# Kernel tuning notes

Measured on AMD Instinct MI355X. Metric: run time of the kernel, lower is better.

The kernel has to match this reference:

```python
import jax, jax.numpy as jnp
import numpy as np

EMBED = 768
HEADS = 12


def setup_inputs() -> dict:
    key = jax.random.key(0)
    k1, k2, k3 = jax.random.split(key, 3)
    B, N, E = 2, 2048, EMBED
    x = jax.random.normal(k1, (B, N, E), dtype=jnp.float32)
    w_qkv = jax.random.normal(k2, (3 * E, E), dtype=jnp.float32) * (1.0 / np.sqrt(E))
    b_qkv = jnp.zeros((3 * E,), dtype=jnp.float32)
    w_o = jax.random.normal(k3, (E, E), dtype=jnp.float32) * (1.0 / np.sqrt(E))
    b_o = jnp.zeros((E,), dtype=jnp.float32)
    return {"x": x, "w_qkv": w_qkv, "b_qkv": b_qkv, "w_o": w_o, "b_o": b_o}


def reference(x, w_qkv, b_qkv, w_o, b_o):
    B, N, E = x.shape
    H = HEADS
    d = E // H
    # fused qkv projection (torch Linear: x @ W^T + b)
    qkv = x @ w_qkv.T + b_qkv                       # [B, N, 3E]
    # Rearrange 'b n (h qkv e) -> b qkv h n e'
    qkv = qkv.reshape(B, N, H, 3, d).transpose(0, 3, 2, 1, 4)  # [B, 3, H, N, d]
    q, k, v = qkv[:, 0], qkv[:, 1], qkv[:, 2]       # each [B, H, N, d]
    scores = jnp.einsum("bhqd,bhkd->bhqk", q, k)    # [B, H, N, N]
    attn = jax.nn.softmax(scores / jnp.sqrt(jnp.float32(E)), axis=-1)
    ctx = jnp.einsum("bhqk,bhkd->bhqd", attn, v)    # [B, H, N, d]
    ctx = ctx.transpose(0, 2, 1, 3).reshape(B, N, E)  # 'b h n d -> b n (h d)'
    out = ctx @ w_o.T + b_o
    return out
```

## Files before the change

### kernel.cpp

```cpp
#include <hip/hip_runtime.h>

#define BB 2
#define NN 2048
#define EE 768
#define HH 12
#define DD 64
#define MM (BB*NN)
#define E3 (3*EE)
#define QSCALE 0.05205877280961602f

typedef __bf16 bf16x8 __attribute__((ext_vector_type(8)));
typedef float  f32x4  __attribute__((ext_vector_type(4)));
typedef unsigned short u16x8 __attribute__((ext_vector_type(8)));

#define MFMA(a,b,c) __builtin_amdgcn_mfma_f32_16x16x32_bf16(a,b,c,0,0,0)

__device__ __forceinline__ unsigned short f2bf(float f) {
    unsigned int u = __float_as_uint(f);
    u += 0x7FFFu + ((u >> 16) & 1u);
    return (unsigned short)(u >> 16);
}

__device__ __forceinline__ bf16x8 as_bf16x8(u16x8 v) {
    union { u16x8 u; bf16x8 b; } c; c.u = v; return c.b;
}

typedef __attribute__((address_space(3))) unsigned int as3u32;
typedef __attribute__((address_space(1))) unsigned int as1u32;
__device__ __forceinline__ void gll16(const void* g, void* l) {
    __builtin_amdgcn_global_load_lds((const as1u32*)(uintptr_t)g,
                                     (as3u32*)(unsigned int)(uintptr_t)l, 16, 0, 0);
}

#define XB4 786432
#define WQ4 442368
#define WO4 147456
__global__ __launch_bounds__(256)
void cast3(const float* __restrict__ x, const float* __restrict__ wq,
           const float* __restrict__ wo, unsigned short* __restrict__ dst) {
    int i = blockIdx.x * 256 + threadIdx.x;
    const float* src;
    int off;
    if (i < XB4)            { src = x;  off = i; }
    else if (i < XB4+WQ4)   { src = wq; off = i - XB4; }
    else                    { src = wo; off = i - XB4 - WQ4; }
    float4 v = ((const float4*)src)[off];
    ushort4 o;
    o.x = f2bf(v.x); o.y = f2bf(v.y); o.z = f2bf(v.z); o.w = f2bf(v.w);
    ((ushort4*)dst)[i] = o;
}

__global__ __launch_bounds__(256)
void gemm_qkv(const unsigned short* __restrict__ A, const unsigned short* __restrict__ W,
              const float* __restrict__ bias,
              unsigned short* __restrict__ o0, unsigned short* __restrict__ o1,
              unsigned short* __restrict__ o2)
{
    __shared__ unsigned short As[128 * 32];
    __shared__ unsigned short Bs[64 * 32];

    const int tid = threadIdx.x;
    const int l = tid & 63;
    const int w = tid >> 6;
    const int m0 = blockIdx.x * 128;
    const int c0 = blockIdx.y * 64;
    const int wm = (w >> 1) * 64;
    const int wn = (w & 1) * 32;

    const unsigned short* s_src[3];
    unsigned short* s_dst[3];
    #pragma unroll
    for (int s = 0; s < 3; ++s) {
        const int ch = 3*w + s;
        if (ch < 8) {
            s_src[s] = A + (size_t)(m0 + ch*16 + (l>>2)) * EE + (l&3)*8;
            s_dst[s] = &As[ch*512];
        } else {
            s_src[s] = W + (size_t)(c0 + (ch-8)*16 + (l>>2)) * EE + (l&3)*8;
            s_dst[s] = &Bs[(ch-8)*512];
        }
    }

    const f32x4 zero4 = {0.f, 0.f, 0.f, 0.f};
    f32x4 acc[4][2];
    #pragma unroll
    for (int i = 0; i < 4; ++i)
        #pragma unroll
        for (int j = 0; j < 2; ++j) acc[i][j] = zero4;

    for (int k0 = 0; k0 < EE; k0 += 32) {
        __syncthreads();
        #pragma unroll
        for (int s = 0; s < 3; ++s) gll16(s_src[s] + k0, s_dst[s]);
        __syncthreads();

        bf16x8 af[4], bf[2];
        #pragma unroll
        for (int i = 0; i < 4; ++i)
            af[i] = *(const bf16x8*)&As[(wm + 16*i + (l&15))*32 + (l>>4)*8];
        #pragma unroll
        for (int j = 0; j < 2; ++j)
            bf[j] = *(const bf16x8*)&Bs[(wn + 16*j + (l&15))*32 + (l>>4)*8];
        #pragma unroll
        for (int i = 0; i < 4; ++i)
            #pragma unroll
            for (int j = 0; j < 2; ++j)
                acc[i][j] = MFMA(af[i], bf[j], acc[i][j]);
    }

    const int sec = c0 >> 6;
    const int hh = sec / 3;
    const int tt = sec - hh*3;
    #pragma unroll
    for (int j = 0; j < 2; ++j) {
        const int col = c0 + wn + 16*j + (l&15);
        const int dcol = wn + 16*j + (l&15);
        const float bj = bias[col];
        #pragma unroll
        for (int i = 0; i < 4; ++i) {
            const int row0 = m0 + wm + 16*i + (l>>4)*4;
            const int b = row0 >> 11;
            const int n = row0 & (NN - 1);
            if (tt == 2) {
                ushort4 pk;
                pk.x = f2bf(acc[i][j][0] + bj);
                pk.y = f2bf(acc[i][j][1] + bj);
                pk.z = f2bf(acc[i][j][2] + bj);
                pk.w = f2bf(acc[i][j][3] + bj);
                *(ushort4*)&o2[(((size_t)b*HH + hh)*DD + dcol)*NN + n] = pk;
            } else {
                unsigned short* dst = (tt == 0) ? o0 : o1;
                #pragma unroll
                for (int r = 0; r < 4; ++r) {
                    float val = acc[i][j][r] + bj;
                    if (tt == 0) val *= QSCALE;
                    dst[(((size_t)b*HH + hh)*NN + n + r)*DD + dcol] = f2bf(val);
                }
            }
        }
    }
}

__global__ __launch_bounds__(256)
void gemm_out(const unsigned short* __restrict__ A, const unsigned short* __restrict__ W,
              const float* __restrict__ bias, float* __restrict__ of)
{
    __shared__ unsigned short As[64 * 32];
    __shared__ unsigned short Bs[64 * 32];

    const int tid = threadIdx.x;
    const int l = tid & 63;
    const int w = tid >> 6;
    const int m0 = blockIdx.x * 64;
    const int c0 = blockIdx.y * 64;
    const int wm = (w >> 1) * 32;
    const int wn = (w & 1) * 32;

    const unsigned short* s_src[2];
    unsigned short* s_dst[2];
    #pragma unroll
    for (int s = 0; s < 2; ++s) {
        const int ch = 2*w + s;
        if (ch < 4) {
            s_src[s] = A + (size_t)(m0 + ch*16 + (l>>2)) * EE + (l&3)*8;
            s_dst[s] = &As[ch*512];
        } else {
            s_src[s] = W + (size_t)(c0 + (ch-4)*16 + (l>>2)) * EE + (l&3)*8;
            s_dst[s] = &Bs[(ch-4)*512];
        }
    }

    const f32x4 zero4 = {0.f, 0.f, 0.f, 0.f};
    f32x4 acc[2][2];
    #pragma unroll
    for (int i = 0; i < 2; ++i)
        #pragma unroll
        for (int j = 0; j < 2; ++j) acc[i][j] = zero4;

    for (int k0 = 0; k0 < EE; k0 += 32) {
        __syncthreads();
        #pragma unroll
        for (int s = 0; s < 2; ++s) gll16(s_src[s] + k0, s_dst[s]);
        __syncthreads();

        bf16x8 af[2], bf[2];
        #pragma unroll
        for (int i = 0; i < 2; ++i)
            af[i] = *(const bf16x8*)&As[(wm + 16*i + (l&15))*32 + (l>>4)*8];
        #pragma unroll
        for (int j = 0; j < 2; ++j)
            bf[j] = *(const bf16x8*)&Bs[(wn + 16*j + (l&15))*32 + (l>>4)*8];
        #pragma unroll
        for (int i = 0; i < 2; ++i)
            #pragma unroll
            for (int j = 0; j < 2; ++j)
                acc[i][j] = MFMA(af[i], bf[j], acc[i][j]);
    }

    #pragma unroll
    for (int j = 0; j < 2; ++j) {
        const int col = c0 + wn + 16*j + (l&15);
        const float bj = bias[col];
        #pragma unroll
        for (int i = 0; i < 2; ++i) {
            #pragma unroll
            for (int r = 0; r < 4; ++r) {
                const int row = m0 + wm + 16*i + (l>>4)*4 + r;
                of[(size_t)row * EE + col] = acc[i][j][r] + bj;
            }
        }
    }
}

struct KVT { u16x8 k0, k1, k2, k3, v0, v1, v2, v3; };

__global__ __launch_bounds__(256)
void attn_mfma(const unsigned short* __restrict__ Q, const unsigned short* __restrict__ K,
               const unsigned short* __restrict__ Vt_g, unsigned short* __restrict__ ctx)
{
    __shared__ unsigned short Ks[2 * 64 * 64];
    __shared__ unsigned short Vt[2 * 64 * 64];

    const int tid = threadIdx.x;
    const int l = tid & 63;
    const int w = tid >> 6;
    const int quad = l >> 4;
    const int lc = l & 15;
    const int x7 = lc & 7;

    const int id = blockIdx.x;
    const int bh = id % 24;
    const int bq = id / 24;
    const int b  = bh / 12;
    const int h  = bh - b*12;
    const size_t hb = (size_t)bh * NN * DD;

    const f32x4 zero4 = {0.f, 0.f, 0.f, 0.f};

    const int qrow = bq*64 + w*16 + lc;
    const bf16x8 qf0 = *(const bf16x8*)(Q + hb + (size_t)qrow*DD +      quad*8);
    const bf16x8 qf1 = *(const bf16x8*)(Q + hb + (size_t)qrow*DD + 32 + quad*8);

    f32x4 o[4];
    #pragma unroll
    for (int dj = 0; dj < 4; ++dj) o[dj] = zero4;
    float lsum = 0.f;

    const int srow = tid >> 2;
    const int sc = tid & 3;
    const unsigned short* kbase = K + hb + (size_t)srow*DD + sc*16;
    const int keyA = (sc & 1)*8 + (sc >> 1)*32;
    const unsigned short* vbase = Vt_g + hb + (size_t)srow*NN + keyA;
    const int c0s = ((2*sc)     ^ (srow & 7)) * 8;
    const int c1s = ((2*sc + 1) ^ (srow & 7)) * 8;
    const int so = srow * 64;

    const int chq0 = ((    quad) ^ x7) * 8;
    const int chq1 = ((4 + quad) ^ x7) * 8;

    auto loadt = [&](KVT& R, int kt) {
        const unsigned short* k0p = kbase + (size_t)kt*128*DD;
        const unsigned short* v0p = vbase + kt*128;
        R.k0 = *(const u16x8*)k0p;
        R.k1 = *(const u16x8*)(k0p + 8);
        R.k2 = *(const u16x8*)(k0p + (size_t)64*DD);
        R.k3 = *(const u16x8*)(k0p + (size_t)64*DD + 8);
        R.v0 = *(const u16x8*)v0p;
        R.v1 = *(const u16x8*)(v0p + 16);
        R.v2 = *(const u16x8*)(v0p + 64);
        R.v3 = *(const u16x8*)(v0p + 64 + 16);
    };

    auto step = [&](KVT& CUR, KVT& NXT, int kt) {
        asm volatile("s_waitcnt lgkmcnt(0)" ::: "memory");
        __builtin_amdgcn_s_barrier();

        u16x8 w0 = __builtin_shufflevector(CUR.v0, CUR.v1, 0,1,2,3, 8,9,10,11);
        u16x8 w1 = __builtin_shufflevector(CUR.v0, CUR.v1, 4,5,6,7, 12,13,14,15);
        u16x8 w2 = __builtin_shufflevector(CUR.v2, CUR.v3, 0,1,2,3, 8,9,10,11);
        u16x8 w3 = __builtin_shufflevector(CUR.v2, CUR.v3, 4,5,6,7, 12,13,14,15);
        *(u16x8*)&Ks[so + c0s]        = CUR.k0;
        *(u16x8*)&Ks[so + c1s]        = CUR.k1;
        *(u16x8*)&Ks[4096 + so + c0s] = CUR.k2;
        *(u16x8*)&Ks[4096 + so + c1s] = CUR.k3;
        *(u16x8*)&Vt[so + c0s]        = w0;
        *(u16x8*)&Vt[so + c1s]        = w1;
        *(u16x8*)&Vt[4096 + so + c0s] = w2;
        *(u16x8*)&Vt[4096 + so + c1s] = w3;

        if (kt + 1 < NN/128) loadt(NXT, kt + 1);

        asm volatile("s_waitcnt lgkmcnt(0)" ::: "memory");
        __builtin_amdgcn_s_barrier();
        __builtin_amdgcn_sched_barrier(0);

        #pragma unroll
        for (int hf = 0; hf < 2; ++hf) {
            const int base = hf * 4096;

            f32x4 st[4];
            #pragma unroll
            for (int jf = 0; jf < 4; ++jf) {
                bf16x8 kf0 = *(const bf16x8*)&Ks[base + (16*jf + lc)*64 + chq0];
                bf16x8 kf1 = *(const bf16x8*)&Ks[base + (16*jf + lc)*64 + chq1];
                f32x4 acc0 = MFMA(kf0, qf0, zero4);
                st[jf] = MFMA(kf1, qf1, acc0);
            }

            f32x4 ev[4];
            #pragma unroll
            for (int jf = 0; jf < 4; ++jf) {
                ev[jf][0] = __builtin_amdgcn_exp2f(st[jf][0]);
                ev[jf][1] = __builtin_amdgcn_exp2f(st[jf][1]);
                ev[jf][2] = __builtin_amdgcn_exp2f(st[jf][2]);
                ev[jf][3] = __builtin_amdgcn_exp2f(st[jf][3]);
                lsum += (ev[jf][0] + ev[jf][1]) + (ev[jf][2] + ev[jf][3]);
            }
            u16x8 p0, p1;
            #pragma unroll
            for (int r = 0; r < 4; ++r) {
                p0[r]     = f2bf(ev[0][r]);
                p0[r + 4] = f2bf(ev[1][r]);
                p1[r]     = f2bf(ev[2][r]);
                p1[r + 4] = f2bf(ev[3][r]);
            }
            const bf16x8 pf0 = as_bf16x8(p0);
            const bf16x8 pf1 = as_bf16x8(p1);

            #pragma unroll
            for (int dj = 0; dj < 4; ++dj) {
                bf16x8 vf0 = *(const bf16x8*)&Vt[base + (16*dj + lc)*64 + chq0];
                bf16x8 vf1 = *(const bf16x8*)&Vt[base + (16*dj + lc)*64 + chq1];
                o[dj] = MFMA(vf0, pf0, o[dj]);
                o[dj] = MFMA(vf1, pf1, o[dj]);
            }
        }
    };

    KVT ra, rb;
    loadt(ra, 0);
    for (int it = 0; it < NN/256; ++it) {
        step(ra, rb, 2*it);
        step(rb, ra, 2*it + 1);
    }

    lsum += __shfl_xor(lsum, 16);
    lsum += __shfl_xor(lsum, 32);
    const float inv = 1.f / lsum;

    const int n = bq*64 + w*16 + lc;
    #pragma unroll
    for (int dj = 0; dj < 4; ++dj) {
        ushort4 pk;
        pk.x = f2bf(o[dj][0] * inv);
        pk.y = f2bf(o[dj][1] * inv);
        pk.z = f2bf(o[dj][2] * inv);
        pk.w = f2bf(o[dj][3] * inv);
        *(ushort4*)&ctx[((size_t)(b*NN + n))*EE + h*DD + 16*dj + quad*4] = pk;
    }
}

extern "C" void kernel_launch(void* const* d_in, const int* in_sizes, int n_in,
                              void* d_out, int out_size, void* d_ws, size_t ws_size,
                              hipStream_t stream)
{
    const float* x     = (const float*)d_in[0];
    const float* w_qkv = (const float*)d_in[1];
    const float* b_qkv = (const float*)d_in[2];
    const float* w_o   = (const float*)d_in[3];
    const float* b_o   = (const float*)d_in[4];
    float* out = (float*)d_out;

    unsigned short* wsu = (unsigned short*)d_ws;
    const size_t XB = (size_t)MM * EE;
    const size_t WQ = (size_t)E3 * EE;
    const size_t WO = (size_t)EE * EE;
    const size_t HS = (size_t)BB * HH * NN * DD;
    unsigned short* xb   = wsu;
    unsigned short* wqb  = xb  + XB;
    unsigned short* wob  = wqb + WQ;
    unsigned short* qb   = wob + WO;
    unsigned short* kb   = qb  + HS;
    unsigned short* vtb  = kb  + HS;
    unsigned short* ctxb = vtb + HS;

    cast3<<<(XB4 + WQ4 + WO4)/256, 256, 0, stream>>>(x, w_qkv, w_o, xb);

    dim3 g1(MM/128, E3/64);
    gemm_qkv<<<g1, 256, 0, stream>>>(xb, wqb, b_qkv, qb, kb, vtb);

    attn_mfma<<<768, 256, 0, stream>>>(qb, kb, vtb, ctxb);

    dim3 g3(MM/64, EE/64);
    gemm_out<<<g3, 256, 0, stream>>>(ctxb, wob, b_o, out);
}
```

Before: 168.5 us.

## Halve attention block to two waves, each handling two 16-row query groups

The attention kernel now runs 128 threads per block, and each wave processes 32 query rows as two 16-row groups. Every K and V fragment read from shared memory therefore feeds two sets of MFMAs, which halves LDS reads per unit of compute and barrier cost per query. Global K/V staging is redistributed so each thread loads 8 vectors per half-tile instead of 4. The trade-off is more registers per thread and fewer waves per block to hide latency.

```diff
diff --git a/kernel.cpp b/kernel.cpp
--- a/kernel.cpp
+++ b/kernel.cpp
@@ -212,9 +212,9 @@
     }
 }
 
-struct KVT { u16x8 k0, k1, k2, k3, v0, v1, v2, v3; };
-
-__global__ __launch_bounds__(256)
+struct KVT { u16x8 k[2][4]; u16x8 v[2][4]; };
+
+__global__ __launch_bounds__(128)
 void attn_mfma(const unsigned short* __restrict__ Q, const unsigned short* __restrict__ K,
                const unsigned short* __restrict__ Vt_g, unsigned short* __restrict__ ctx)
 {
@@ -237,56 +237,67 @@
 
     const f32x4 zero4 = {0.f, 0.f, 0.f, 0.f};
 
-    const int qrow = bq*64 + w*16 + lc;
-    const bf16x8 qf0 = *(const bf16x8*)(Q + hb + (size_t)qrow*DD +      quad*8);
-    const bf16x8 qf1 = *(const bf16x8*)(Q + hb + (size_t)qrow*DD + 32 + quad*8);
-
-    f32x4 o[4];
-    #pragma unroll
-    for (int dj = 0; dj < 4; ++dj) o[dj] = zero4;
-    float lsum = 0.f;
-
-    const int srow = tid >> 2;
-    const int sc = tid & 3;
-    const unsigned short* kbase = K + hb + (size_t)srow*DD + sc*16;
-    const int keyA = (sc & 1)*8 + (sc >> 1)*32;
-    const unsigned short* vbase = Vt_g + hb + (size_t)srow*NN + keyA;
-    const int c0s = ((2*sc)     ^ (srow & 7)) * 8;
-    const int c1s = ((2*sc + 1) ^ (srow & 7)) * 8;
+    bf16x8 qf0[2], qf1[2];
+    #pragma unroll
+    for (int qg = 0; qg < 2; ++qg) {
+        const int qrow = bq*64 + w*32 + qg*16 + lc;
+        qf0[qg] = *(const bf16x8*)(Q + hb + (size_t)qrow*DD +      quad*8);
+        qf1[qg] = *(const bf16x8*)(Q + hb + (size_t)qrow*DD + 32 + quad*8);
+    }
+
+    f32x4 o[2][4];
+    #pragma unroll
+    for (int qg = 0; qg < 2; ++qg)
+        #pragma unroll
+        for (int dj = 0; dj < 4; ++dj) o[qg][dj] = zero4;
+    float lsum[2] = {0.f, 0.f};
+
+    const int srow = tid >> 1;
+    const int sc = tid & 1;
+    const unsigned short* kbase = K + hb + (size_t)srow*DD + sc*32;
+    const unsigned short* vbase = Vt_g + hb + (size_t)srow*NN + sc*32;
+    const int sw = srow & 7;
+    int coff[4];
+    #pragma unroll
+    for (int i = 0; i < 4; ++i) coff[i] = ((4*sc + i) ^ sw) * 8;
     const int so = srow * 64;
 
     const int chq0 = ((    quad) ^ x7) * 8;
     const int chq1 = ((4 + quad) ^ x7) * 8;
 
     auto loadt = [&](KVT& R, int kt) {
-        const unsigned short* k0p = kbase + (size_t)kt*128*DD;
-        const unsigned short* v0p = vbase + kt*128;
-        R.k0 = *(const u16x8*)k0p;
-        R.k1 = *(const u16x8*)(k0p + 8);
-        R.k2 = *(const u16x8*)(k0p + (size_t)64*DD);
-        R.k3 = *(const u16x8*)(k0p + (size_t)64*DD + 8);
-        R.v0 = *(const u16x8*)v0p;
-        R.v1 = *(const u16x8*)(v0p + 16);
-        R.v2 = *(const u16x8*)(v0p + 64);
-        R.v3 = *(const u16x8*)(v0p + 64 + 16);
+        #pragma unroll
+        for (int hf = 0; hf < 2; ++hf) {
+            const unsigned short* kp = kbase + ((size_t)kt*128 + 64*hf)*DD;
+            const unsigned short* vp = vbase + kt*128 + 64*hf;
+            #pragma unroll
+            for (int i = 0; i < 4; ++i) {
+                R.k[hf][i] = *(const u16x8*)(kp + i*8);
+                R.v[hf][i] = *(const u16x8*)(vp + i*8);
+            }
+        }
     };
 
     auto step = [&](KVT& CUR, KVT& NXT, int kt) {
         asm volatile("s_waitcnt lgkmcnt(0)" ::: "memory");
         __builtin_amdgcn_s_barrier();
 
-        u16x8 w0 = __builtin_shufflevector(CUR.v0, CUR.v1, 0,1,2,3, 8,9,10,11);
-        u16x8 w1 = __builtin_shufflevector(CUR.v0, CUR.v1, 4,5,6,7, 12,13,14,15);
-        u16x8 w2 = __builtin_shufflevector(CUR.v2, CUR.v3, 0,1,2,3, 8,9,10,11);
-        u16x8 w3 = __builtin_shufflevector(CUR.v2, CUR.v3, 4,5,6,7, 12,13,14,15);
-        *(u16x8*)&Ks[so + c0s]        = CUR.k0;
-        *(u16x8*)&Ks[so + c1s]        = CUR.k1;
-        *(u16x8*)&Ks[4096 + so + c0s] = CUR.k2;
-        *(u16x8*)&Ks[4096 + so + c1s] = CUR.k3;
-        *(u16x8*)&Vt[so + c0s]        = w0;
-        *(u16x8*)&Vt[so + c1s]        = w1;
-        *(u16x8*)&Vt[4096 + so + c0s] = w2;
-        *(u16x8*)&Vt[4096 + so + c1s] = w3;
+        #pragma unroll
+        for (int hf = 0; hf < 2; ++hf) {
+            const int hb4 = hf*4096 + so;
+            *(u16x8*)&Ks[hb4 + coff[0]] = CUR.k[hf][0];
+            *(u16x8*)&Ks[hb4 + coff[1]] = CUR.k[hf][1];
+            *(u16x8*)&Ks[hb4 + coff[2]] = CUR.k[hf][2];
+            *(u16x8*)&Ks[hb4 + coff[3]] = CUR.k[hf][3];
+            u16x8 w0 = __builtin_shufflevector(CUR.v[hf][0], CUR.v[hf][2], 0,1,2,3, 8,9,10,11);
+            u16x8 w1 = __builtin_shufflevector(CUR.v[hf][0], CUR.v[hf][2], 4,5,6,7, 12,13,14,15);
+            u16x8 w2 = __builtin_shufflevector(CUR.v[hf][1], CUR.v[hf][3], 0,1,2,3, 8,9,10,11);
+            u16x8 w3 = __builtin_shufflevector(CUR.v[hf][1], CUR.v[hf][3], 4,5,6,7, 12,13,14,15);
+            *(u16x8*)&Vt[hb4 + coff[0]] = w0;
+            *(u16x8*)&Vt[hb4 + coff[1]] = w1;
+            *(u16x8*)&Vt[hb4 + coff[2]] = w2;
+            *(u16x8*)&Vt[hb4 + coff[3]] = w3;
+        }
 
         if (kt + 1 < NN/128) loadt(NXT, kt + 1);
 
@@ -298,41 +309,51 @@
         for (int hf = 0; hf < 2; ++hf) {
             const int base = hf * 4096;
 
-            f32x4 st[4];
+            f32x4 st[2][4];
             #pragma unroll
             for (int jf = 0; jf < 4; ++jf) {
                 bf16x8 kf0 = *(const bf16x8*)&Ks[base + (16*jf + lc)*64 + chq0];
                 bf16x8 kf1 = *(const bf16x8*)&Ks[base + (16*jf + lc)*64 + chq1];
-                f32x4 acc0 = MFMA(kf0, qf0, zero4);
-                st[jf] = MFMA(kf1, qf1, acc0);
-            }
-
-            f32x4 ev[4];
-            #pragma unroll
-            for (int jf = 0; jf < 4; ++jf) {
-                ev[jf][0] = __builtin_amdgcn_exp2f(st[jf][0]);
-                ev[jf][1] = __builtin_amdgcn_exp2f(st[jf][1]);
-                ev[jf][2] = __builtin_amdgcn_exp2f(st[jf][2]);
-                ev[jf][3] = __builtin_amdgcn_exp2f(st[jf][3]);
-                lsum += (ev[jf][0] + ev[jf][1]) + (ev[jf][2] + ev[jf][3]);
-            }
-            u16x8 p0, p1;
-            #pragma unroll
-            for (int r = 0; r < 4; ++r) {
-                p0[r]     = f2bf(ev[0][r]);
-                p0[r + 4] = f2bf(ev[1][r]);
-                p1[r]     = f2bf(ev[2][r]);
-                p1[r + 4] = f2bf(ev[3][r]);
-            }
-            const bf16x8 pf0 = as_bf16x8(p0);
-            const bf16x8 pf1 = as_bf16x8(p1);
+                #pragma unroll
+                for (int qg = 0; qg < 2; ++qg) {
+                    f32x4 acc0 = MFMA(kf0, qf0[qg], zero4);
+                    st[qg][jf] = MFMA(kf1, qf1[qg], acc0);
+                }
+            }
+
+            bf16x8 pf0[2], pf1[2];
+            #pragma unroll
+            for (int qg = 0; qg < 2; ++qg) {
+                f32x4 ev[4];
+                #pragma unroll
+                for (int jf = 0; jf < 4; ++jf) {
+                    ev[jf][0] = __builtin_amdgcn_exp2f(st[qg][jf][0]);
+                    ev[jf][1] = __builtin_amdgcn_exp2f(st[qg][jf][1]);
+                    ev[jf][2] = __builtin_amdgcn_exp2f(st[qg][jf][2]);
+                    ev[jf][3] = __builtin_amdgcn_exp2f(st[qg][jf][3]);
+                    lsum[qg] += (ev[jf][0] + ev[jf][1]) + (ev[jf][2] + ev[jf][3]);
+                }
+                u16x8 p0, p1;
+                #pragma unroll
+                for (int r = 0; r < 4; ++r) {
+                    p0[r]     = f2bf(ev[0][r]);
+                    p0[r + 4] = f2bf(ev[1][r]);
+                    p1[r]     = f2bf(ev[2][r]);
+                    p1[r + 4] = f2bf(ev[3][r]);
+                }
+                pf0[qg] = as_bf16x8(p0);
+                pf1[qg] = as_bf16x8(p1);
+            }
 
             #pragma unroll
             for (int dj = 0; dj < 4; ++dj) {
                 bf16x8 vf0 = *(const bf16x8*)&Vt[base + (16*dj + lc)*64 + chq0];
                 bf16x8 vf1 = *(const bf16x8*)&Vt[base + (16*dj + lc)*64 + chq1];
-                o[dj] = MFMA(vf0, pf0, o[dj]);
-                o[dj] = MFMA(vf1, pf1, o[dj]);
+                #pragma unroll
+                for (int qg = 0; qg < 2; ++qg) {
+                    o[qg][dj] = MFMA(vf0, pf0[qg], o[qg][dj]);
+                    o[qg][dj] = MFMA(vf1, pf1[qg], o[qg][dj]);
+                }
             }
         }
     };
@@ -344,19 +365,22 @@
         step(rb, ra, 2*it + 1);
     }
 
-    lsum += __shfl_xor(lsum, 16);
-    lsum += __shfl_xor(lsum, 32);
-    const float inv = 1.f / lsum;
-
-    const int n = bq*64 + w*16 + lc;
-    #pragma unroll
-    for (int dj = 0; dj < 4; ++dj) {
-        ushort4 pk;
-        pk.x = f2bf(o[dj][0] * inv);
-        pk.y = f2bf(o[dj][1] * inv);
-        pk.z = f2bf(o[dj][2] * inv);
-        pk.w = f2bf(o[dj][3] * inv);
-        *(ushort4*)&ctx[((size_t)(b*NN + n))*EE + h*DD + 16*dj + quad*4] = pk;
+    #pragma unroll
+    for (int qg = 0; qg < 2; ++qg) {
+        float s = lsum[qg];
+        s += __shfl_xor(s, 16);
+        s += __shfl_xor(s, 32);
+        const float inv = 1.f / s;
+        const int n = bq*64 + w*32 + qg*16 + lc;
+        #pragma unroll
+        for (int dj = 0; dj < 4; ++dj) {
+            ushort4 pk;
+            pk.x = f2bf(o[qg][dj][0] * inv);
+            pk.y = f2bf(o[qg][dj][1] * inv);
+            pk.z = f2bf(o[qg][dj][2] * inv);
+            pk.w = f2bf(o[qg][dj][3] * inv);
+            *(ushort4*)&ctx[((size_t)(b*NN + n))*EE + h*DD + 16*dj + quad*4] = pk;
+        }
     }
 }
 
@@ -389,7 +413,7 @@
     dim3 g1(MM/128, E3/64);
     gemm_qkv<<<g1, 256, 0, stream>>>(xb, wqb, b_qkv, qb, kb, vtb);
 
-    attn_mfma<<<768, 256, 0, stream>>>(qb, kb, vtb, ctxb);
+    attn_mfma<<<768, 128, 0, stream>>>(qb, kb, vtb, ctxb);
 
     dim3 g3(MM/64, EE/64);
     gemm_out<<<g3, 256, 0, stream>>>(ctxb, wob, b_o, out);
```

After: 184.2 us. 1.09x slower.

## Split attention over key dimension and add combine kernel

Applied to the files above, without the earlier changes.

Splits each attention block's key range into two halves across a second grid dimension, doubling the block count from 768 to 1536 so more CUs stay busy. Each split writes unnormalized fp32 partial outputs and row sums, and a new combine kernel adds them, normalizes and writes bf16 context. This adds an extra launch plus fp32 partial-output traffic through global memory. A launch-bounds occupancy hint of 5 blocks is also added. The merge adds the partial outputs directly without any max rescaling, so it relies on the softmax numerator having no running-max subtraction.

```diff
diff --git a/kernel.cpp b/kernel.cpp
--- a/kernel.cpp
+++ b/kernel.cpp
@@ -7,6 +7,8 @@
 #define DD 64
 #define MM (BB*NN)
 #define E3 (3*EE)
+#define NSPLIT 2
+#define KEYS_PER_SPLIT (NN/NSPLIT)
 #define QSCALE 0.05205877280961602f
 
 typedef __bf16 bf16x8 __attribute__((ext_vector_type(8)));
@@ -214,9 +216,10 @@
 
 struct KVT { u16x8 k0, k1, k2, k3, v0, v1, v2, v3; };
 
-__global__ __launch_bounds__(256)
+__global__ __launch_bounds__(256, 5)
 void attn_mfma(const unsigned short* __restrict__ Q, const unsigned short* __restrict__ K,
-               const unsigned short* __restrict__ Vt_g, unsigned short* __restrict__ ctx)
+               const unsigned short* __restrict__ Vt_g,
+               float* __restrict__ Opart, float* __restrict__ Lpart)
 {
     __shared__ unsigned short Ks[2 * 64 * 64];
     __shared__ unsigned short Vt[2 * 64 * 64];
@@ -229,10 +232,9 @@
     const int x7 = lc & 7;
 
     const int id = blockIdx.x;
+    const int sp = blockIdx.y;
     const int bh = id % 24;
     const int bq = id / 24;
-    const int b  = bh / 12;
-    const int h  = bh - b*12;
     const size_t hb = (size_t)bh * NN * DD;
 
     const f32x4 zero4 = {0.f, 0.f, 0.f, 0.f};
@@ -248,9 +250,9 @@
 
     const int srow = tid >> 2;
     const int sc = tid & 3;
-    const unsigned short* kbase = K + hb + (size_t)srow*DD + sc*16;
+    const unsigned short* kbase = K + hb + (size_t)(sp*KEYS_PER_SPLIT + srow)*DD + sc*16;
     const int keyA = (sc & 1)*8 + (sc >> 1)*32;
-    const unsigned short* vbase = Vt_g + hb + (size_t)srow*NN + keyA;
+    const unsigned short* vbase = Vt_g + hb + (size_t)srow*NN + sp*KEYS_PER_SPLIT + keyA;
     const int c0s = ((2*sc)     ^ (srow & 7)) * 8;
     const int c1s = ((2*sc + 1) ^ (srow & 7)) * 8;
     const int so = srow * 64;
@@ -288,7 +290,7 @@
         *(u16x8*)&Vt[4096 + so + c0s] = w2;
         *(u16x8*)&Vt[4096 + so + c1s] = w3;
 
-        if (kt + 1 < NN/128) loadt(NXT, kt + 1);
+        if (kt + 1 < KEYS_PER_SPLIT/128) loadt(NXT, kt + 1);
 
         asm volatile("s_waitcnt lgkmcnt(0)" ::: "memory");
         __builtin_amdgcn_s_barrier();
@@ -339,25 +341,44 @@
 
     KVT ra, rb;
     loadt(ra, 0);
-    for (int it = 0; it < NN/256; ++it) {
+    for (int it = 0; it < KEYS_PER_SPLIT/256; ++it) {
         step(ra, rb, 2*it);
         step(rb, ra, 2*it + 1);
     }
 
     lsum += __shfl_xor(lsum, 16);
     lsum += __shfl_xor(lsum, 32);
-    const float inv = 1.f / lsum;
 
     const int n = bq*64 + w*16 + lc;
-    #pragma unroll
-    for (int dj = 0; dj < 4; ++dj) {
-        ushort4 pk;
-        pk.x = f2bf(o[dj][0] * inv);
-        pk.y = f2bf(o[dj][1] * inv);
-        pk.z = f2bf(o[dj][2] * inv);
-        pk.w = f2bf(o[dj][3] * inv);
-        *(ushort4*)&ctx[((size_t)(b*NN + n))*EE + h*DD + 16*dj + quad*4] = pk;
-    }
+    float* op = Opart + ((size_t)(sp*24 + bh)*NN + n)*DD + quad*4;
+    #pragma unroll
+    for (int dj = 0; dj < 4; ++dj)
+        *(f32x4*)(op + 16*dj) = o[dj];
+    if (quad == 0)
+        Lpart[(size_t)(sp*24 + bh)*NN + n] = lsum;
+}
+
+#define RTOT (24*NN)
+__global__ __launch_bounds__(256)
+void combine(const float* __restrict__ Op, const float* __restrict__ Lp,
+             unsigned short* __restrict__ ctx)
+{
+    const int t = blockIdx.x * 256 + threadIdx.x;
+    const int r = t >> 4;
+    const int c = t & 15;
+    const float4 a = *(const float4*)&Op[(size_t)r*DD + c*4];
+    const float4 bv = *(const float4*)&Op[((size_t)RTOT + r)*DD + c*4];
+    const float inv = 1.f / (Lp[r] + Lp[RTOT + r]);
+    const int bh = r >> 11;
+    const int n = r & (NN - 1);
+    const int b = bh / 12;
+    const int h = bh - b*12;
+    ushort4 pk;
+    pk.x = f2bf((a.x + bv.x) * inv);
+    pk.y = f2bf((a.y + bv.y) * inv);
+    pk.z = f2bf((a.z + bv.z) * inv);
+    pk.w = f2bf((a.w + bv.w) * inv);
+    *(ushort4*)&ctx[((size_t)(b*NN + n))*EE + h*DD + c*4] = pk;
 }
 
 extern "C" void kernel_launch(void* const* d_in, const int* in_sizes, int n_in,
@@ -383,13 +404,18 @@
     unsigned short* kb   = qb  + HS;
     unsigned short* vtb  = kb  + HS;
     unsigned short* ctxb = vtb + HS;
+    float* opart = (float*)(ctxb + HS);
+    float* lpart = opart + (size_t)NSPLIT * 24 * NN * DD;
 
     cast3<<<(XB4 + WQ4 + WO4)/256, 256, 0, stream>>>(x, w_qkv, w_o, xb);
 
     dim3 g1(MM/128, E3/64);
     gemm_qkv<<<g1, 256, 0, stream>>>(xb, wqb, b_qkv, qb, kb, vtb);
 
-    attn_mfma<<<768, 256, 0, stream>>>(qb, kb, vtb, ctxb);
+    dim3 g2(768, NSPLIT);
+    attn_mfma<<<g2, 256, 0, stream>>>(qb, kb, vtb, opart, lpart);
+
+    combine<<<(RTOT*16)/256, 256, 0, stream>>>(opart, lpart, ctxb);
 
     dim3 g3(MM/64, EE/64);
     gemm_out<<<g3, 256, 0, stream>>>(ctxb, wob, b_o, out);
```

Result: slower. 259.8 us (+54.2%).
